# Optimization experiments

Measured on AMD Instinct MI355X. Metric: run time of the kernel, lower is better.

Reference implementation:

```python
import jax, jax.numpy as jnp
import numpy as np

DIM = 768
N_HEADS = 12
HEAD_DIM = DIM // N_HEADS
HIDDEN = 4 * DIM
EPS = 1e-5


def _layernorm(x, g, b):
    m = jnp.mean(x, axis=-1, keepdims=True)
    v = jnp.mean(jnp.square(x - m), axis=-1, keepdims=True)
    return (x - m) * jax.lax.rsqrt(v + EPS) * g + b


def setup_inputs() -> dict:
    key = jax.random.key(0)
    ks = jax.random.split(key, 16)
    s = lambda fan_in: 1.0 / np.sqrt(fan_in)
    return {
        "x": jax.random.normal(ks[0], (2, 2048, DIM), dtype=jnp.float32),
        "ln1_g": jnp.ones((DIM,), jnp.float32),
        "ln1_b": jnp.zeros((DIM,), jnp.float32),
        "qkv_w": jax.random.uniform(ks[1], (DIM, 3 * DIM), jnp.float32, -s(DIM), s(DIM)),
        "qkv_b": jax.random.uniform(ks[2], (3 * DIM,), jnp.float32, -s(DIM), s(DIM)),
        "proj_w": jax.random.uniform(ks[3], (DIM, DIM), jnp.float32, -s(DIM), s(DIM)),
        "proj_b": jax.random.uniform(ks[4], (DIM,), jnp.float32, -s(DIM), s(DIM)),
        "ln2_g": jnp.ones((DIM,), jnp.float32),
        "ln2_b": jnp.zeros((DIM,), jnp.float32),
        "w1": jax.random.uniform(ks[5], (DIM, HIDDEN), jnp.float32, -s(DIM), s(DIM)),
        "b1": jax.random.uniform(ks[6], (HIDDEN,), jnp.float32, -s(DIM), s(DIM)),
        "w2": jax.random.uniform(ks[7], (HIDDEN, DIM), jnp.float32, -s(HIDDEN), s(HIDDEN)),
        "b2": jax.random.uniform(ks[8], (DIM,), jnp.float32, -s(HIDDEN), s(HIDDEN)),
    }


def reference(x, ln1_g, ln1_b, qkv_w, qkv_b, proj_w, proj_b, ln2_g, ln2_b, w1, b1, w2, b2):
    B, N, C = x.shape
    # ---- attention branch (pre-norm) ----
    h = _layernorm(x, ln1_g, ln1_b)
    qkv = (h @ qkv_w + qkv_b).reshape(B, N, 3, N_HEADS, HEAD_DIM)
    qkv = qkv.transpose(2, 0, 3, 1, 4)  # [3, B, H, N, Dh]
    q, k, v = qkv[0], qkv[1], qkv[2]
    scale = HEAD_DIM ** -0.5
    scores = jnp.einsum("bhnd,bhmd->bhnm", q, k) * scale  # [B,H,N,N]
    attn = jax.nn.softmax(scores, axis=-1)
    ctx = jnp.einsum("bhnm,bhmd->bhnd", attn, v)  # [B,H,N,Dh]
    ctx = ctx.transpose(0, 2, 1, 3).reshape(B, N, C)
    x = x + ctx @ proj_w + proj_b
    # ---- MLP branch (pre-norm) ----
    h = _layernorm(x, ln2_g, ln2_b)
    h = jax.nn.gelu(h @ w1 + b1, approximate=False)  # torch nn.GELU default = exact erf
    x = x + h @ w2 + b2
    return x
```

## Files before the change

### kernel.cpp

```cpp
#include <hip/hip_runtime.h>
#include <hip/hip_bf16.h>
#include <math.h>

#define DIM 768
#define NHEADS 12
#define HDIM 64
#define HIDDEN 3072
#define SEQ 2048
#define NTOK 4096
#define QKV3 2304

typedef __attribute__((ext_vector_type(8))) __bf16 bf16x8;
typedef __attribute__((ext_vector_type(4))) float f32x4;
typedef __attribute__((ext_vector_type(16))) float f32x16;

__device__ __forceinline__ ushort f32_bf16(float f) {
  union { float f; uint u; } c{f};
  uint u = c.u;
  u = (u + 0x7FFFu + ((u >> 16) & 1u)) >> 16;
  return (ushort)u;
}

__device__ __forceinline__ float bf16_f32(ushort u) {
  union { uint u; float f; } c{(uint)u << 16};
  return c.f;
}

__device__ __forceinline__ uint cvt_pk_bf16(float lo, float hi) {
  uint r;
  asm("v_cvt_pk_bf16_f32 %0, %1, %2" : "=v"(r) : "v"(lo), "v"(hi));
  return r;
}

#define EXP2F(x) __builtin_amdgcn_exp2f(x)

__device__ __forceinline__ void glds16(const ushort* g, ushort* l) {
  __builtin_amdgcn_global_load_lds(
      (const __attribute__((address_space(1))) unsigned int*)(const void*)g,
      (__attribute__((address_space(3))) unsigned int*)(void*)l, 16, 0, 0);
}

union U8 { uint u[4]; bf16x8 v; };

__global__ __launch_bounds__(256) void prep_kernel(
    const float* __restrict__ qkv_w, const float* __restrict__ proj_w,
    const float* __restrict__ w1, const float* __restrict__ w2,
    ushort* __restrict__ o0, ushort* __restrict__ o1,
    ushort* __restrict__ o2, ushort* __restrict__ o3,
    const float* __restrict__ x, const float* __restrict__ g1,
    const float* __restrict__ b1v, ushort* __restrict__ lnout) {
  int bid = blockIdx.x;
  int t = threadIdx.x;
  if (bid < 6912) {
    __shared__ float tile[32][33];
    const float* in; ushort* out; int K, N;
    if (bid < 1728)      { in = qkv_w;  out = o0; K = DIM;    N = QKV3; }
    else if (bid < 2304) { bid -= 1728; in = proj_w; out = o1; K = DIM;  N = DIM; }
    else if (bid < 4608) { bid -= 2304; in = w1;  out = o2; K = DIM;    N = HIDDEN; }
    else                 { bid -= 4608; in = w2;  out = o3; K = HIDDEN; N = DIM; }
    int ntx = N / 32;
    int nb = (bid % ntx) * 32, kb = (bid / ntx) * 32;
    int tx = t & 31, ty = t >> 5;
#pragma unroll
    for (int i = 0; i < 32; i += 8)
      tile[ty + i][tx] = in[(size_t)(kb + ty + i) * N + nb + tx];
    __syncthreads();
#pragma unroll
    for (int i = 0; i < 32; i += 8)
      out[(size_t)(nb + ty + i) * K + kb + tx] = f32_bf16(tile[tx][ty + i]);
  } else {
    int row = bid - 6912;
    const float* xr = x + (size_t)row * DIM;
    float v0 = xr[t], v1 = xr[t + 256], v2 = xr[t + 512];
    float s = v0 + v1 + v2;
    float q = v0 * v0 + v1 * v1 + v2 * v2;
#pragma unroll
    for (int m = 1; m < 64; m <<= 1) {
      s += __shfl_xor(s, m);
      q += __shfl_xor(q, m);
    }
    __shared__ float ss[4], qq[4];
    int wid = t >> 6;
    if ((t & 63) == 0) { ss[wid] = s; qq[wid] = q; }
    __syncthreads();
    s = ss[0] + ss[1] + ss[2] + ss[3];
    q = qq[0] + qq[1] + qq[2] + qq[3];
    float mean = s * (1.0f / DIM);
    float var = q * (1.0f / DIM) - mean * mean;
    float rs = rsqrtf(var + 1e-5f);
    size_t o = (size_t)row * DIM;
    lnout[o + t]       = f32_bf16((v0 - mean) * rs * g1[t]       + b1v[t]);
    lnout[o + t + 256] = f32_bf16((v1 - mean) * rs * g1[t + 256] + b1v[t + 256]);
    lnout[o + t + 512] = f32_bf16((v2 - mean) * rs * g1[t + 512] + b1v[t + 512]);
  }
}

template <int EPI>
__global__ __launch_bounds__(256, 4) void gemm_bf16(
    const ushort* __restrict__ A, const ushort* __restrict__ Bt,
    const float* __restrict__ bias, const float* __restrict__ resid,
    void* __restrict__ outv, int M, int N, int K, int lda, int ldb,
    ushort* __restrict__ p0, ushort* __restrict__ p1, ushort* __restrict__ p2) {
  __shared__ __align__(16) ushort As[128 * 64];
  __shared__ __align__(16) ushort Bs[128 * 64];
  int t = threadIdx.x;
  int lane = t & 63, w = t >> 6;
  int wr = w >> 1, wc = w & 1;
  int nxy = gridDim.x * gridDim.y;
  int flat = blockIdx.x + gridDim.x * blockIdx.y;
  int swz = (flat & 7) * (nxy >> 3) + (flat >> 3);
  int m0 = (swz / gridDim.x) * 128, n0 = (swz % gridDim.x) * 128;
  int kb = blockIdx.z * K;
  f32x4 acc[4][4] = {};
  int rl = lane & 15, g = lane >> 4, rl7 = rl & 7;

  int baseRow = w * 32 + (lane >> 3);
  int cs = (lane & 7) ^ ((lane >> 3) & 7);
  const ushort* Asrc = A + (size_t)(m0 + baseRow) * lda + kb + cs * 8;
  const ushort* Bsrc = Bt + (size_t)(n0 + baseRow) * ldb + kb + cs * 8;
  ushort* Adst = &As[(w * 256 + lane) * 8];
  ushort* Bdst = &Bs[(w * 256 + lane) * 8];

  for (int k0 = 0; k0 < K; k0 += 64) {
    __syncthreads();
#pragma unroll
    for (int i = 0; i < 4; i++) {
      glds16(Asrc + (size_t)i * 8 * lda + k0, Adst + i * 512);
      glds16(Bsrc + (size_t)i * 8 * ldb + k0, Bdst + i * 512);
    }
    __syncthreads();
    bf16x8 a[2][4], b[2][4];
#pragma unroll
    for (int kk = 0; kk < 2; kk++)
#pragma unroll
      for (int i = 0; i < 4; i++) {
        a[kk][i] = *(const bf16x8*)&As[(wr * 64 + i * 16 + rl) * 64 + ((kk * 4 + g) ^ rl7) * 8];
        b[kk][i] = *(const bf16x8*)&Bs[(wc * 64 + i * 16 + rl) * 64 + ((kk * 4 + g) ^ rl7) * 8];
      }
#pragma unroll
    for (int kk = 0; kk < 2; kk++)
#pragma unroll
      for (int i = 0; i < 4; i++)
#pragma unroll
        for (int j = 0; j < 4; j++)
          acc[i][j] = __builtin_amdgcn_mfma_f32_16x16x32_bf16(a[kk][i], b[kk][j], acc[i][j], 0, 0, 0);
  }
  ushort* pz = (blockIdx.z == 0) ? p0 : ((blockIdx.z == 1) ? p1 : p2);
  int g4 = (lane >> 4) * 4;
#pragma unroll
  for (int i = 0; i < 4; i++) {
#pragma unroll
    for (int j = 0; j < 4; j++) {
      int col = n0 + wc * 64 + j * 16 + rl;
      float bval = (EPI == 3) ? 0.0f : bias[col];
#pragma unroll
      for (int r = 0; r < 4; r++) {
        int row = m0 + wr * 64 + i * 16 + g4 + r;
        float v = acc[i][j][r] + bval;
        if (EPI == 0) {
          ushort val = f32_bf16(v);
          if (col < 2 * DIM) {
            ((ushort*)outv)[(size_t)row * N + col] = val;
          } else {
            int hv = (col - 2 * DIM) >> 6, dd = (col - 2 * DIM) & 63;
            p0[((size_t)((row >> 11) * NHEADS + hv) * 64 + dd) * SEQ + (row & (SEQ - 1))] = val;
          }
        } else if (EPI == 1) {
          v += resid[(size_t)row * N + col];
          ((float*)outv)[(size_t)row * N + col] = v;
        } else if (EPI == 2) {
          float e = EXP2F(-2.4554593f * v);
          v = v * __builtin_amdgcn_rcpf(1.0f + e);
          ((ushort*)outv)[(size_t)row * N + col] = f32_bf16(v);
        } else {
          pz[(size_t)row * N + col] = f32_bf16(v);
        }
      }
    }
  }
}

__global__ __launch_bounds__(256) void reduceLN_kernel(
    const ushort* __restrict__ p0, const ushort* __restrict__ p1,
    const ushort* __restrict__ p2, const float* __restrict__ x,
    const float* __restrict__ bias, const float* __restrict__ g,
    const float* __restrict__ bta, float* __restrict__ x1,
    ushort* __restrict__ lnout) {
  int row = blockIdx.x;
  int t = threadIdx.x;
  size_t base4 = (size_t)row * (DIM / 4);
  float4 val = {0, 0, 0, 0};
  float s = 0.0f, q = 0.0f;
  if (t < DIM / 4) {
    ushort4 a0 = ((const ushort4*)p0)[base4 + t];
    ushort4 a1 = ((const ushort4*)p1)[base4 + t];
    ushort4 a2 = ((const ushort4*)p2)[base4 + t];
    float4 xv = ((const float4*)x)[base4 + t];
    const float4 bv = ((const float4*)bias)[t];
    val.x = xv.x + bv.x + bf16_f32(a0.x) + bf16_f32(a1.x) + bf16_f32(a2.x);
    val.y = xv.y + bv.y + bf16_f32(a0.y) + bf16_f32(a1.y) + bf16_f32(a2.y);
    val.z = xv.z + bv.z + bf16_f32(a0.z) + bf16_f32(a1.z) + bf16_f32(a2.z);
    val.w = xv.w + bv.w + bf16_f32(a0.w) + bf16_f32(a1.w) + bf16_f32(a2.w);
    ((float4*)x1)[base4 + t] = val;
    s = (val.x + val.y) + (val.z + val.w);
    q = (val.x * val.x + val.y * val.y) + (val.z * val.z + val.w * val.w);
  }
#pragma unroll
  for (int m = 1; m < 64; m <<= 1) {
    s += __shfl_xor(s, m);
    q += __shfl_xor(q, m);
  }
  __shared__ float ss[4], qq[4];
  int wid = t >> 6;
  if ((t & 63) == 0) { ss[wid] = s; qq[wid] = q; }
  __syncthreads();
  s = ss[0] + ss[1] + ss[2];
  q = qq[0] + qq[1] + qq[2];
  float mean = s * (1.0f / DIM);
  float var = q * (1.0f / DIM) - mean * mean;
  float rs = rsqrtf(var + 1e-5f);
  if (t < DIM / 4) {
    const float4 gv = ((const float4*)g)[t];
    const float4 btv = ((const float4*)bta)[t];
    ushort4 o;
    o.x = f32_bf16((val.x - mean) * rs * gv.x + btv.x);
    o.y = f32_bf16((val.y - mean) * rs * gv.y + btv.y);
    o.z = f32_bf16((val.z - mean) * rs * gv.z + btv.z);
    o.w = f32_bf16((val.w - mean) * rs * gv.w + btv.w);
    ((ushort4*)lnout)[base4 + t] = o;
  }
}

__global__ __launch_bounds__(256) void reduce3_kernel(
    const ushort* __restrict__ p0, const ushort* __restrict__ p1,
    const ushort* __restrict__ p2, const float* __restrict__ x1,
    const float* __restrict__ bias, float* __restrict__ out) {
  int i = blockIdx.x * 256 + threadIdx.x;
  int col = (i * 4) % DIM;
  const ushort4 a0 = ((const ushort4*)p0)[i];
  const ushort4 a1 = ((const ushort4*)p1)[i];
  const ushort4 a2 = ((const ushort4*)p2)[i];
  const float4 xv = ((const float4*)x1)[i];
  const float4 bv = *(const float4*)&bias[col];
  float4 o;
  o.x = xv.x + bv.x + bf16_f32(a0.x) + bf16_f32(a1.x) + bf16_f32(a2.x);
  o.y = xv.y + bv.y + bf16_f32(a0.y) + bf16_f32(a1.y) + bf16_f32(a2.y);
  o.z = xv.z + bv.z + bf16_f32(a0.z) + bf16_f32(a1.z) + bf16_f32(a2.z);
  o.w = xv.w + bv.w + bf16_f32(a0.w) + bf16_f32(a1.w) + bf16_f32(a2.w);
  ((float4*)out)[i] = o;
}

__global__ __launch_bounds__(256, 3) void attn_kernel(
    const ushort* __restrict__ qkv, const ushort* __restrict__ vT,
    ushort* __restrict__ ctx) {
  __shared__ __align__(16) ushort Ks[128 * 64];
  __shared__ __align__(16) ushort Vt[64 * 128];
  __shared__ float mml[2][64];
  int t = threadIdx.x, lane = t & 63, w = t >> 6;
  int qh = w & 1, kvpar = w >> 1;
  int kl = lane & 31, hi = lane >> 5;
  int i0 = blockIdx.x;
  int xcd = i0 & 7, j = i0 >> 3;
  int qt = j & 31, grp = j >> 5;
  int pair = xcd + 8 * grp;
  int h = pair % 12, b = pair / 12;

  bf16x8 bq[4];
  {
    size_t qbase = (size_t)(b * SEQ + qt * 64 + qh * 32 + kl) * QKV3 + h * HDIM + hi * 8;
#pragma unroll
    for (int mi = 0; mi < 4; mi++) bq[mi] = *(const bf16x8*)(qkv + qbase + mi * 16);
#pragma unroll
    for (int mi = 0; mi < 4; mi++)
#pragma unroll
      for (int e = 0; e < 8; e++)
        bq[mi][e] = (__bf16)((float)bq[mi][e] * 0.18033688f);
  }
  f32x16 acc_o[2] = {};
  float lst = 0.0f;

  const ushort* kbase = qkv + (size_t)(b * SEQ) * QKV3 + DIM + h * HDIM;
  const ushort* vtb = vT + (size_t)(b * NHEADS + h) * 64 * SEQ;

  for (int kt = 0; kt < SEQ / 128; kt++) {
    __syncthreads();
#pragma unroll
    for (int i = 0; i < 4; i++) {
      int s = i * 256 + t;
      int krow = s >> 3, kcc = s & 7;
      glds16(kbase + (size_t)(kt * 128 + krow) * QKV3 + ((kcc ^ (krow & 7)) * 8),
             &Ks[s * 8]);
      int vrow = s >> 4, vcc = s & 15;
      glds16(vtb + (size_t)vrow * SEQ + kt * 128 + ((vcc ^ (vrow & 15)) * 8),
             &Vt[s * 8]);
    }
    __syncthreads();

    f32x16 accs[2] = {};
#pragma unroll
    for (int ks = 0; ks < 2; ks++) {
      int key = kvpar * 64 + ks * 32 + kl;
#pragma unroll
      for (int mi = 0; mi < 4; mi++) {
        bf16x8 ak = *(const bf16x8*)&Ks[key * 64 + (((2 * mi + hi) ^ (key & 7)) * 8)];
        accs[ks] = __builtin_amdgcn_mfma_f32_32x32x16_bf16(ak, bq[mi], accs[ks], 0, 0, 0);
      }
    }

    float psv[4] = {0.0f, 0.0f, 0.0f, 0.0f};
    uint PK[2][8];
#pragma unroll
    for (int ks = 0; ks < 2; ks++)
#pragma unroll
      for (int rp = 0; rp < 8; rp++) {
        float p0 = EXP2F(accs[ks][2 * rp]);
        float p1 = EXP2F(accs[ks][2 * rp + 1]);
        psv[rp & 3] += p0 + p1;
        PK[ks][rp] = cvt_pk_bf16(p0, p1);
      }
    float ps = (psv[0] + psv[1]) + (psv[2] + psv[3]);
    ps += __shfl_xor(ps, 32);
    lst += ps;

#pragma unroll
    for (int tt = 0; tt < 4; tt++) {
      const int ks = tt >> 1, tb = 4 * (tt & 1);
      uint e0 = hi ? PK[ks][tb]     : PK[ks][tb + 2];
      uint e1 = hi ? PK[ks][tb + 1] : PK[ks][tb + 3];
      uint x0 = __shfl_xor(e0, 32), x1 = __shfl_xor(e1, 32);
      uint l0 = hi ? PK[ks][tb + 2] : PK[ks][tb];
      uint l1 = hi ? PK[ks][tb + 3] : PK[ks][tb + 1];
      U8 a;
      a.u[0] = hi ? x0 : l0;
      a.u[1] = hi ? x1 : l1;
      a.u[2] = hi ? l0 : x0;
      a.u[3] = hi ? l1 : x1;
      int chunk = kvpar * 8 + 2 * tt + hi;
#pragma unroll
      for (int dn = 0; dn < 2; dn++) {
        int d = dn * 32 + kl;
        bf16x8 bv = *(const bf16x8*)&Vt[d * 128 + ((chunk ^ (d & 15)) * 8)];
        acc_o[dn] = __builtin_amdgcn_mfma_f32_32x32x16_bf16(a.v, bv, acc_o[dn], 0, 0, 0);
      }
    }
  }

  __syncthreads();
  float* obuf = ((float*)Ks) + qh * 2048;
  if (kvpar == 1) {
#pragma unroll
    for (int dn = 0; dn < 2; dn++)
#pragma unroll
      for (int r = 0; r < 16; r++)
        obuf[(dn * 16 + r) * 64 + lane] = acc_o[dn][r];
    mml[qh][lane] = lst;
  }
  __syncthreads();
  if (kvpar == 0) {
    lst += mml[qh][lane];
    float inv = 1.0f / lst;
#pragma unroll
    for (int r = 0; r < 16; r++) {
      int qrow = (r & 3) + 8 * (r >> 2) + 4 * hi;
      int src = qrow | (lane & 32);
      float ir = __shfl(inv, src);
      size_t row = (size_t)(b * SEQ + qt * 64 + qh * 32 + qrow);
#pragma unroll
      for (int dn = 0; dn < 2; dn++) {
        float v = (acc_o[dn][r] + obuf[(dn * 16 + r) * 64 + lane]) * ir;
        ctx[row * DIM + h * HDIM + dn * 32 + kl] = f32_bf16(v);
      }
    }
  }
}

extern "C" void kernel_launch(void* const* d_in, const int* in_sizes, int n_in,
                              void* d_out, int out_size, void* d_ws, size_t ws_size,
                              hipStream_t stream) {
  const float* x      = (const float*)d_in[0];
  const float* ln1_g  = (const float*)d_in[1];
  const float* ln1_b  = (const float*)d_in[2];
  const float* qkv_w  = (const float*)d_in[3];
  const float* qkv_b  = (const float*)d_in[4];
  const float* proj_w = (const float*)d_in[5];
  const float* proj_b = (const float*)d_in[6];
  const float* ln2_g  = (const float*)d_in[7];
  const float* ln2_b  = (const float*)d_in[8];
  const float* w1     = (const float*)d_in[9];
  const float* b1     = (const float*)d_in[10];
  const float* w2     = (const float*)d_in[11];
  const float* b2     = (const float*)d_in[12];
  float* out = (float*)d_out;

  char* ws = (char*)d_ws;
  size_t off = 0;
  auto alloc = [&](size_t bytes) -> void* {
    void* p = ws + off;
    off += (bytes + 255) & ~(size_t)255;
    return p;
  };
  ushort* wqkv_t  = (ushort*)alloc((size_t)QKV3 * DIM * 2);
  ushort* wproj_t = (ushort*)alloc((size_t)DIM * DIM * 2);
  ushort* w1_t    = (ushort*)alloc((size_t)HIDDEN * DIM * 2);
  ushort* w2_t    = (ushort*)alloc((size_t)DIM * HIDDEN * 2);
  ushort* hbuf    = (ushort*)alloc((size_t)NTOK * DIM * 2);
  ushort* ubuf    = (ushort*)alloc((size_t)NTOK * HIDDEN * 2);
  ushort* ctx     = (ushort*)alloc((size_t)NTOK * DIM * 2);
  float*  x1      = (float*)alloc((size_t)NTOK * DIM * 4);
  ushort* qkvbuf = ubuf;
  ushort* m1     = ubuf;
  ushort* vT = (ushort*)x1;
  ushort* pp0 = ubuf;
  ushort* pp1 = ubuf + (size_t)NTOK * DIM;
  ushort* pp2 = ubuf + (size_t)2 * NTOK * DIM;
  ushort* part0 = (ushort*)ws;
  ushort* part1 = hbuf;
  ushort* part2 = ctx;

  prep_kernel<<<6912 + NTOK, 256, 0, stream>>>(
      qkv_w, proj_w, w1, w2, wqkv_t, wproj_t, w1_t, w2_t,
      x, ln1_g, ln1_b, hbuf);

  gemm_bf16<0><<<dim3(QKV3 / 128, NTOK / 128), 256, 0, stream>>>(
      hbuf, wqkv_t, qkv_b, nullptr, qkvbuf, NTOK, QKV3, DIM, DIM, DIM,
      vT, nullptr, nullptr);
  attn_kernel<<<768, 256, 0, stream>>>(qkvbuf, vT, ctx);
  gemm_bf16<3><<<dim3(DIM / 128, NTOK / 128, 3), 256, 0, stream>>>(
      ctx, wproj_t, nullptr, nullptr, nullptr, NTOK, DIM, DIM / 3, DIM, DIM,
      pp0, pp1, pp2);
  reduceLN_kernel<<<NTOK, 256, 0, stream>>>(
      pp0, pp1, pp2, x, proj_b, ln2_g, ln2_b, x1, hbuf);
  gemm_bf16<2><<<dim3(HIDDEN / 128, NTOK / 128), 256, 0, stream>>>(
      hbuf, w1_t, b1, nullptr, m1, NTOK, HIDDEN, DIM, DIM, DIM,
      nullptr, nullptr, nullptr);
  gemm_bf16<3><<<dim3(DIM / 128, NTOK / 128, 3), 256, 0, stream>>>(
      m1, w2_t, nullptr, nullptr, nullptr, NTOK, DIM, HIDDEN / 3, HIDDEN, HIDDEN,
      part0, part1, part2);
  reduce3_kernel<<<NTOK * DIM / 4 / 256, 256, 0, stream>>>(
      part0, part1, part2, x1, b2, out);
}
```

Baseline: 173.1 us.

## Replace split-K partial buffers and reduce kernel with fp32 atomic accumulation

The final MLP down-projection split-K GEMM now atomically adds its fp32 partial sums straight into the output. The output is pre-initialised with residual plus b2 inside the LayerNorm-reduce kernel, so the separate reduce3 kernel and its partial-buffer traffic are removed. This also avoids rounding each partial to bf16. In exchange it adds atomic-add traffic, the summation order becomes nondeterministic, and the LN kernel writes an extra output. The bf16 conversion helper is also switched to the compiler's native cast.

Result: slower. 188.1 us (+8.7%).

```diff
diff --git a/kernel.cpp b/kernel.cpp
--- a/kernel.cpp
+++ b/kernel.cpp
@@ -15,10 +15,9 @@
 typedef __attribute__((ext_vector_type(16))) float f32x16;
 
 __device__ __forceinline__ ushort f32_bf16(float f) {
-  union { float f; uint u; } c{f};
-  uint u = c.u;
-  u = (u + 0x7FFFu + ((u >> 16) & 1u)) >> 16;
-  return (ushort)u;
+  __bf16 h = (__bf16)f;
+  union { __bf16 h; ushort u; } c{h};
+  return c.u;
 }
 
 __device__ __forceinline__ float bf16_f32(ushort u) {
@@ -152,7 +151,7 @@
 #pragma unroll
     for (int j = 0; j < 4; j++) {
       int col = n0 + wc * 64 + j * 16 + rl;
-      float bval = (EPI == 3) ? 0.0f : bias[col];
+      float bval = (EPI == 3 || EPI == 4) ? 0.0f : bias[col];
 #pragma unroll
       for (int r = 0; r < 4; r++) {
         int row = m0 + wr * 64 + i * 16 + g4 + r;
@@ -172,8 +171,10 @@
           float e = EXP2F(-2.4554593f * v);
           v = v * __builtin_amdgcn_rcpf(1.0f + e);
           ((ushort*)outv)[(size_t)row * N + col] = f32_bf16(v);
+        } else if (EPI == 3) {
+          pz[(size_t)row * N + col] = f32_bf16(v);
         } else {
-          pz[(size_t)row * N + col] = f32_bf16(v);
+          unsafeAtomicAdd(&((float*)outv)[(size_t)row * N + col], v);
         }
       }
     }
@@ -184,8 +185,9 @@
     const ushort* __restrict__ p0, const ushort* __restrict__ p1,
     const ushort* __restrict__ p2, const float* __restrict__ x,
     const float* __restrict__ bias, const float* __restrict__ g,
-    const float* __restrict__ bta, float* __restrict__ x1,
-    ushort* __restrict__ lnout) {
+    const float* __restrict__ bta, const float* __restrict__ b2,
+    float* __restrict__ x1, ushort* __restrict__ lnout,
+    float* __restrict__ outinit) {
   int row = blockIdx.x;
   int t = threadIdx.x;
   size_t base4 = (size_t)row * (DIM / 4);
@@ -202,6 +204,9 @@
     val.z = xv.z + bv.z + bf16_f32(a0.z) + bf16_f32(a1.z) + bf16_f32(a2.z);
     val.w = xv.w + bv.w + bf16_f32(a0.w) + bf16_f32(a1.w) + bf16_f32(a2.w);
     ((float4*)x1)[base4 + t] = val;
+    const float4 b2v = ((const float4*)b2)[t];
+    float4 oi = {val.x + b2v.x, val.y + b2v.y, val.z + b2v.z, val.w + b2v.w};
+    ((float4*)outinit)[base4 + t] = oi;
     s = (val.x + val.y) + (val.z + val.w);
     q = (val.x * val.x + val.y * val.y) + (val.z * val.z + val.w * val.w);
   }
@@ -229,25 +234,6 @@
     o.w = f32_bf16((val.w - mean) * rs * gv.w + btv.w);
     ((ushort4*)lnout)[base4 + t] = o;
   }
-}
-
-__global__ __launch_bounds__(256) void reduce3_kernel(
-    const ushort* __restrict__ p0, const ushort* __restrict__ p1,
-    const ushort* __restrict__ p2, const float* __restrict__ x1,
-    const float* __restrict__ bias, float* __restrict__ out) {
-  int i = blockIdx.x * 256 + threadIdx.x;
-  int col = (i * 4) % DIM;
-  const ushort4 a0 = ((const ushort4*)p0)[i];
-  const ushort4 a1 = ((const ushort4*)p1)[i];
-  const ushort4 a2 = ((const ushort4*)p2)[i];
-  const float4 xv = ((const float4*)x1)[i];
-  const float4 bv = *(const float4*)&bias[col];
-  float4 o;
-  o.x = xv.x + bv.x + bf16_f32(a0.x) + bf16_f32(a1.x) + bf16_f32(a2.x);
-  o.y = xv.y + bv.y + bf16_f32(a0.y) + bf16_f32(a1.y) + bf16_f32(a2.y);
-  o.z = xv.z + bv.z + bf16_f32(a0.z) + bf16_f32(a1.z) + bf16_f32(a2.z);
-  o.w = xv.w + bv.w + bf16_f32(a0.w) + bf16_f32(a1.w) + bf16_f32(a2.w);
-  ((float4*)out)[i] = o;
 }
 
 __global__ __launch_bounds__(256, 3) void attn_kernel(
@@ -413,9 +399,6 @@
   ushort* pp0 = ubuf;
   ushort* pp1 = ubuf + (size_t)NTOK * DIM;
   ushort* pp2 = ubuf + (size_t)2 * NTOK * DIM;
-  ushort* part0 = (ushort*)ws;
-  ushort* part1 = hbuf;
-  ushort* part2 = ctx;
 
   prep_kernel<<<6912 + NTOK, 256, 0, stream>>>(
       qkv_w, proj_w, w1, w2, wqkv_t, wproj_t, w1_t, w2_t,
@@ -429,13 +412,11 @@
       ctx, wproj_t, nullptr, nullptr, nullptr, NTOK, DIM, DIM / 3, DIM, DIM,
       pp0, pp1, pp2);
   reduceLN_kernel<<<NTOK, 256, 0, stream>>>(
-      pp0, pp1, pp2, x, proj_b, ln2_g, ln2_b, x1, hbuf);
+      pp0, pp1, pp2, x, proj_b, ln2_g, ln2_b, b2, x1, hbuf, out);
   gemm_bf16<2><<<dim3(HIDDEN / 128, NTOK / 128), 256, 0, stream>>>(
       hbuf, w1_t, b1, nullptr, m1, NTOK, HIDDEN, DIM, DIM, DIM,
       nullptr, nullptr, nullptr);
-  gemm_bf16<3><<<dim3(DIM / 128, NTOK / 128, 3), 256, 0, stream>>>(
-      m1, w2_t, nullptr, nullptr, nullptr, NTOK, DIM, HIDDEN / 3, HIDDEN, HIDDEN,
-      part0, part1, part2);
-  reduce3_kernel<<<NTOK * DIM / 4 / 256, 256, 0, stream>>>(
-      part0, part1, part2, x1, b2, out);
-}
+  gemm_bf16<4><<<dim3(DIM / 128, NTOK / 128, 3), 256, 0, stream>>>(
+      m1, w2_t, nullptr, nullptr, out, NTOK, DIM, HIDDEN / 3, HIDDEN, HIDDEN,
+      nullptr, nullptr, nullptr);
+}
```
